# Performance work log

Measured on AMD Instinct MI355X. Metric: run time of the kernel, lower is better.

## Reference

```python
import jax, jax.numpy as jnp
import numpy as np

MODE_STATIC = 0
MODE_APPEARANCE_CHANGE = 2
MODE_BLINK = 3
MODE_AFFINE = 4


def _affine_warp(src, theta):
    """F.affine_grid + F.grid_sample(bilinear, zeros, align_corners=False).

    src:   [N, C, H, W]
    theta: [N, 2, 3]
    """
    N, C, H, W = src.shape
    dt = src.dtype
    # affine_grid base coords (align_corners=False): centers of pixels in [-1, 1]
    xs = (jnp.arange(W, dtype=dt) * 2 + 1) / W - 1  # [W]
    ys = (jnp.arange(H, dtype=dt) * 2 + 1) / H - 1  # [H]
    gx = (theta[:, 0, 0][:, None, None] * xs[None, None, :]
          + theta[:, 0, 1][:, None, None] * ys[None, :, None]
          + theta[:, 0, 2][:, None, None])  # [N, H, W]
    gy = (theta[:, 1, 0][:, None, None] * xs[None, None, :]
          + theta[:, 1, 1][:, None, None] * ys[None, :, None]
          + theta[:, 1, 2][:, None, None])  # [N, H, W]
    # unnormalize (align_corners=False)
    ix = ((gx + 1) * W - 1) / 2
    iy = ((gy + 1) * H - 1) / 2
    x0 = jnp.floor(ix)
    y0 = jnp.floor(iy)
    wx1 = ix - x0
    wy1 = iy - y0
    wx0 = 1 - wx1
    wy0 = 1 - wy1
    x0i = x0.astype(jnp.int32)
    y0i = y0.astype(jnp.int32)

    src_flat = src.reshape(N, C, H * W)

    def gather(xi, yi):
        valid = (xi >= 0) & (xi < W) & (yi >= 0) & (yi < H)  # zeros padding
        xi_c = jnp.clip(xi, 0, W - 1)
        yi_c = jnp.clip(yi, 0, H - 1)
        idx = (yi_c * W + xi_c).reshape(N, 1, H * W)
        v = jnp.take_along_axis(src_flat, idx, axis=2).reshape(N, C, H, W)
        return v * valid.astype(dt)[:, None]

    out = (gather(x0i, y0i) * (wx0 * wy0)[:, None]
           + gather(x0i + 1, y0i) * (wx1 * wy0)[:, None]
           + gather(x0i, y0i + 1) * (wx0 * wy1)[:, None]
           + gather(x0i + 1, y0i + 1) * (wx1 * wy1)[:, None])
    return out


def setup_inputs() -> dict:
    key = jax.random.key(0)
    ks = jax.random.split(key, 7)
    B, NI, C, H, W = 4, 16, 3, 256, 256
    g0 = jax.random.normal(ks[0], (B, NI, C, H, W), dtype=jnp.float32)
    m0 = jax.random.uniform(ks[1], (B, NI, 1, H, W), dtype=jnp.float32)
    mode_logits = jax.random.normal(ks[2], (B, NI, 5), dtype=jnp.float32)
    # near-identity affine transforms (realistic small motions)
    ident = jnp.array([1.0, 0.0, 0.0, 0.0, 1.0, 0.0], dtype=jnp.float32)
    transform_params = ident + 0.1 * jax.random.normal(ks[3], (B, NI, 6), dtype=jnp.float32)
    alpha = jax.random.uniform(ks[4], (B, NI, 1), dtype=jnp.float32)
    instance_valid = (jax.random.uniform(ks[5], (B, NI)) > 0.2).astype(jnp.float32)
    i_bg = jax.random.normal(ks[6], (B, C, H, W), dtype=jnp.float32)
    return {"g0": g0, "m0": m0, "mode_logits": mode_logits,
            "transform_params": transform_params, "alpha": alpha,
            "instance_valid": instance_valid, "i_bg": i_bg}


def reference(g0, m0, mode_logits, transform_params, alpha, instance_valid, i_bg):
    B, NI, C, H, W = g0.shape
    theta = transform_params.reshape(-1, 2, 3)  # [B*NI, 2, 3]
    warped_overlay = _affine_warp(g0.reshape(B * NI, C, H, W), theta).reshape(B, NI, C, H, W)
    warped_mask = _affine_warp(m0.reshape(B * NI, 1, H, W), theta).reshape(B, NI, 1, H, W)

    mode_ids = jnp.argmax(mode_logits, axis=-1)  # [B, NI]
    static_like = ((mode_ids == MODE_STATIC) | (mode_ids == MODE_APPEARANCE_CHANGE)
                   | (mode_ids == MODE_AFFINE)).astype(g0.dtype)[:, :, None, None, None]
    blink = (mode_ids == MODE_BLINK).astype(g0.dtype)[:, :, None, None, None]
    alpha_map = alpha[:, :, :, None, None]  # [B, NI, 1, 1, 1]
    valid = instance_valid[:, :, None, None, None]

    g_mid_per_instance = (static_like * warped_overlay + blink * warped_overlay * alpha_map) * valid
    m_mid_per_instance = (static_like * warped_mask + blink * warped_mask * alpha_map) * valid
    g_mid = g_mid_per_instance.sum(axis=1)
    m_mid = jnp.clip(m_mid_per_instance.sum(axis=1), 0.0, 1.0)
    i_base = i_bg + g_mid
    return (g_mid_per_instance, m_mid_per_instance, g_mid, m_mid, i_base)
```

## Files before the change

kernel.cpp:

```cpp
#include <hip/hip_runtime.h>
#include <hip/hip_bf16.h>

#define BB 4
#define NI 16
#define CC 3
#define HH 256
#define WW 256
#define HWSZ (HH * WW)

__global__ void prep_kernel(const float* __restrict__ mode_logits,
                            const float* __restrict__ tp,
                            const float* __restrict__ alpha,
                            const float* __restrict__ iv,
                            float* __restrict__ inst) {
    int i = threadIdx.x;
    if (i >= BB * NI) return;
    float best = mode_logits[i * 5];
    int bid = 0;
#pragma unroll
    for (int k = 1; k < 5; ++k) {
        float v = mode_logits[i * 5 + k];
        if (v > best) { best = v; bid = k; }
    }
    float coef;
    if (bid == 0 || bid == 2 || bid == 4)      coef = 1.0f;
    else if (bid == 3)                          coef = alpha[i];
    else                                        coef = 0.0f;
    coef *= iv[i];
#pragma unroll
    for (int k = 0; k < 6; ++k) inst[i * 8 + k] = tp[i * 6 + k];
    inst[i * 8 + 6] = coef;
    inst[i * 8 + 7] = 0.0f;
}

__global__ __launch_bounds__(256) void warp_main(
    const float* __restrict__ g0,
    const float* __restrict__ m0,
    const float* __restrict__ i_bg,
    const float* __restrict__ inst,
    float* __restrict__ out_gpi,
    float* __restrict__ out_mpi,
    float* __restrict__ out_gmid,
    float* __restrict__ out_mmid,
    float* __restrict__ out_ibase) {
    const int w = threadIdx.x;
    const int h = blockIdx.x;
    const int b = blockIdx.y;
    const int pix = h * WW + w;

    const float xs = (2 * w + 1) * (1.0f / WW) - 1.0f;
    const float ys = (2 * h + 1) * (1.0f / HH) - 1.0f;

    float acc[CC] = {0.f, 0.f, 0.f};
    float accm = 0.f;

    for (int ii = 0; ii < NI; ++ii) {
        const int id = b * NI + ii;
        const float* p = inst + id * 8;
        const float coef = p[6];

        float* gp = out_gpi + (size_t)id * CC * HWSZ + pix;
        float* mp = out_mpi + (size_t)id * HWSZ + pix;

        if (coef == 0.0f) {
            gp[0] = 0.0f; gp[HWSZ] = 0.0f; gp[2 * HWSZ] = 0.0f; mp[0] = 0.0f;
            continue;
        }

        const float gx = p[0] * xs + p[1] * ys + p[2];
        const float gy = p[3] * xs + p[4] * ys + p[5];
        const float ix = gx * (0.5f * WW) + (0.5f * WW - 0.5f);
        const float iy = gy * (0.5f * HH) + (0.5f * HH - 0.5f);
        const float x0f = floorf(ix), y0f = floorf(iy);
        const float wx1 = ix - x0f, wy1 = iy - y0f;
        const float wx0 = 1.0f - wx1, wy0 = 1.0f - wy1;
        const int x0 = (int)x0f, y0 = (int)y0f;
        const bool vx0 = (unsigned)x0 < (unsigned)WW;
        const bool vx1 = (unsigned)(x0 + 1) < (unsigned)WW;
        const bool vy0 = (unsigned)y0 < (unsigned)HH;
        const bool vy1 = (unsigned)(y0 + 1) < (unsigned)HH;
        const bool v00 = vx0 && vy0, v10 = vx1 && vy0;
        const bool v01 = vx0 && vy1, v11 = vx1 && vy1;
        const int o00 = y0 * WW + x0;
        const float w00 = wx0 * wy0, w10 = wx1 * wy0;
        const float w01 = wx0 * wy1, w11 = wx1 * wy1;

        const float* gsrc = g0 + (size_t)id * CC * HWSZ;
        const float* msrc = m0 + (size_t)id * HWSZ;

#pragma unroll
        for (int c = 0; c < CC; ++c) {
            const float* s = gsrc + c * HWSZ;
            const float a00 = v00 ? s[o00] : 0.0f;
            const float a10 = v10 ? s[o00 + 1] : 0.0f;
            const float a01 = v01 ? s[o00 + WW] : 0.0f;
            const float a11 = v11 ? s[o00 + WW + 1] : 0.0f;
            const float val = coef * (w00 * a00 + w10 * a10 + w01 * a01 + w11 * a11);
            gp[c * HWSZ] = val;
            acc[c] += val;
        }
        {
            const float a00 = v00 ? msrc[o00] : 0.0f;
            const float a10 = v10 ? msrc[o00 + 1] : 0.0f;
            const float a01 = v01 ? msrc[o00 + WW] : 0.0f;
            const float a11 = v11 ? msrc[o00 + WW + 1] : 0.0f;
            const float val = coef * (w00 * a00 + w10 * a10 + w01 * a01 + w11 * a11);
            mp[0] = val;
            accm += val;
        }
    }

    const int ob = b * CC * HWSZ + pix;
#pragma unroll
    for (int c = 0; c < CC; ++c) {
        out_gmid[ob + c * HWSZ] = acc[c];
        out_ibase[ob + c * HWSZ] = acc[c] + i_bg[ob + c * HWSZ];
    }
    out_mmid[b * HWSZ + pix] = fminf(fmaxf(accm, 0.0f), 1.0f);
}

extern "C" void kernel_launch(void* const* d_in, const int* in_sizes, int n_in,
                              void* d_out, int out_size, void* d_ws, size_t ws_size,
                              hipStream_t stream) {
    const float* g0          = (const float*)d_in[0];
    const float* m0          = (const float*)d_in[1];
    const float* mode_logits = (const float*)d_in[2];
    const float* tp          = (const float*)d_in[3];
    const float* alpha       = (const float*)d_in[4];
    const float* iv          = (const float*)d_in[5];
    const float* i_bg        = (const float*)d_in[6];

    float* out       = (float*)d_out;
    float* out_gpi   = out;
    float* out_mpi   = out_gpi  + (size_t)BB * NI * CC * HWSZ;
    float* out_gmid  = out_mpi  + (size_t)BB * NI * HWSZ;
    float* out_mmid  = out_gmid + (size_t)BB * CC * HWSZ;
    float* out_ibase = out_mmid + (size_t)BB * HWSZ;

    float* inst = (float*)d_ws;

    prep_kernel<<<1, 64, 0, stream>>>(mode_logits, tp, alpha, iv, inst);

    dim3 grid(HH, BB);
    warp_main<<<grid, WW, 0, stream>>>(g0, m0, i_bg, inst,
                                       out_gpi, out_mpi, out_gmid, out_mmid, out_ibase);
}
```

Before: 164.8 us.

## Split instance loop into two halves with partial sums and combine kernel

The per-batch instance loop is split across two grid z-slices, and each slice writes float4 partial sums to workspace. A separate combine kernel then adds the halves and produces g_mid, m_mid and i_base. The prep kernel now builds compacted lists of active instances, so the warp kernel skips zero-coefficient instances without branching per instance, and all gather loads are hoisted for more memory-level parallelism. This doubles the block count to improve occupancy, at the cost of an extra launch and partial-sum traffic; a fused fallback is kept for when workspace is too small.

```diff
diff --git a/kernel.cpp b/kernel.cpp
--- a/kernel.cpp
+++ b/kernel.cpp
@@ -1,5 +1,4 @@
 #include <hip/hip_runtime.h>
-#include <hip/hip_bf16.h>
 
 #define BB 4
 #define NI 16
@@ -7,65 +6,72 @@
 #define HH 256
 #define WW 256
 #define HWSZ (HH * WW)
-
-__global__ void prep_kernel(const float* __restrict__ mode_logits,
+#define HALF (NI / 2)
+
+
+__global__ void prep_kernel(const float* __restrict__ ml,
                             const float* __restrict__ tp,
-                            const float* __restrict__ alpha,
+                            const float* __restrict__ al,
                             const float* __restrict__ iv,
-                            float* __restrict__ inst) {
-    int i = threadIdx.x;
-    if (i >= BB * NI) return;
-    float best = mode_logits[i * 5];
+                            float* __restrict__ wsf) {
+    __shared__ float scoef[BB * NI];
+    const int i = threadIdx.x;
+    float best = ml[i * 5];
     int bid = 0;
 #pragma unroll
     for (int k = 1; k < 5; ++k) {
-        float v = mode_logits[i * 5 + k];
+        float v = ml[i * 5 + k];
         if (v > best) { best = v; bid = k; }
     }
-    float coef;
-    if (bid == 0 || bid == 2 || bid == 4)      coef = 1.0f;
-    else if (bid == 3)                          coef = alpha[i];
-    else                                        coef = 0.0f;
+    float coef = (bid == 0 || bid == 2 || bid == 4) ? 1.0f
+               : (bid == 3 ? al[i] : 0.0f);
     coef *= iv[i];
 #pragma unroll
-    for (int k = 0; k < 6; ++k) inst[i * 8 + k] = tp[i * 6 + k];
-    inst[i * 8 + 6] = coef;
-    inst[i * 8 + 7] = 0.0f;
-}
-
-__global__ __launch_bounds__(256) void warp_main(
+    for (int k = 0; k < 6; ++k) wsf[i * 8 + k] = tp[i * 6 + k];
+    wsf[i * 8 + 6] = coef;
+    wsf[i * 8 + 7] = 0.0f;
+    scoef[i] = coef;
+    __syncthreads();
+    if (i < BB * 2) {
+        const int b = i >> 1, half = i & 1;
+        int* wsi = (int*)(wsf + 512);
+        int cnt = 0;
+#pragma unroll
+        for (int k = 0; k < HALF; ++k) {
+            const int ii = half * HALF + k;
+            if (scoef[b * NI + ii] != 0.0f) wsi[8 + i * 8 + cnt++] = ii;
+        }
+        wsi[i] = cnt;
+    }
+}
+
+__global__ __launch_bounds__(256) void warp_half(
     const float* __restrict__ g0,
     const float* __restrict__ m0,
-    const float* __restrict__ i_bg,
-    const float* __restrict__ inst,
+    const float* __restrict__ wsf,
     float* __restrict__ out_gpi,
     float* __restrict__ out_mpi,
-    float* __restrict__ out_gmid,
-    float* __restrict__ out_mmid,
-    float* __restrict__ out_ibase) {
+    float* __restrict__ part) {
     const int w = threadIdx.x;
     const int h = blockIdx.x;
     const int b = blockIdx.y;
+    const int half = blockIdx.z;
     const int pix = h * WW + w;
 
     const float xs = (2 * w + 1) * (1.0f / WW) - 1.0f;
     const float ys = (2 * h + 1) * (1.0f / HH) - 1.0f;
 
-    float acc[CC] = {0.f, 0.f, 0.f};
-    float accm = 0.f;
-
-    for (int ii = 0; ii < NI; ++ii) {
+    const int* wsi = (const int*)(wsf + 512);
+    const int lk = b * 2 + half;
+    const int nact = wsi[lk];
+    const int* act = wsi + 8 + lk * 8;
+
+    float acc0 = 0.f, acc1 = 0.f, acc2 = 0.f, accm = 0.f;
+
+    auto proc = [&](int ii) {
         const int id = b * NI + ii;
-        const float* p = inst + id * 8;
+        const float* p = wsf + id * 8;
         const float coef = p[6];
-
-        float* gp = out_gpi + (size_t)id * CC * HWSZ + pix;
-        float* mp = out_mpi + (size_t)id * HWSZ + pix;
-
-        if (coef == 0.0f) {
-            gp[0] = 0.0f; gp[HWSZ] = 0.0f; gp[2 * HWSZ] = 0.0f; mp[0] = 0.0f;
-            continue;
-        }
 
         const float gx = p[0] * xs + p[1] * ys + p[2];
         const float gy = p[3] * xs + p[4] * ys + p[5];
@@ -87,29 +93,122 @@
 
         const float* gsrc = g0 + (size_t)id * CC * HWSZ;
         const float* msrc = m0 + (size_t)id * HWSZ;
-
+        float* gp = out_gpi + (size_t)id * CC * HWSZ + pix;
+
+        const float a00_0 = v00 ? gsrc[o00] : 0.0f;
+        const float a10_0 = v10 ? gsrc[o00 + 1] : 0.0f;
+        const float a01_0 = v01 ? gsrc[o00 + WW] : 0.0f;
+        const float a11_0 = v11 ? gsrc[o00 + WW + 1] : 0.0f;
+        const float a00_1 = v00 ? gsrc[HWSZ + o00] : 0.0f;
+        const float a10_1 = v10 ? gsrc[HWSZ + o00 + 1] : 0.0f;
+        const float a01_1 = v01 ? gsrc[HWSZ + o00 + WW] : 0.0f;
+        const float a11_1 = v11 ? gsrc[HWSZ + o00 + WW + 1] : 0.0f;
+        const float a00_2 = v00 ? gsrc[2 * HWSZ + o00] : 0.0f;
+        const float a10_2 = v10 ? gsrc[2 * HWSZ + o00 + 1] : 0.0f;
+        const float a01_2 = v01 ? gsrc[2 * HWSZ + o00 + WW] : 0.0f;
+        const float a11_2 = v11 ? gsrc[2 * HWSZ + o00 + WW + 1] : 0.0f;
+        const float m00 = v00 ? msrc[o00] : 0.0f;
+        const float m10 = v10 ? msrc[o00 + 1] : 0.0f;
+        const float m01 = v01 ? msrc[o00 + WW] : 0.0f;
+        const float m11 = v11 ? msrc[o00 + WW + 1] : 0.0f;
+
+        const float val0 = coef * (w00 * a00_0 + w10 * a10_0 + w01 * a01_0 + w11 * a11_0);
+        const float val1 = coef * (w00 * a00_1 + w10 * a10_1 + w01 * a01_1 + w11 * a11_1);
+        const float val2 = coef * (w00 * a00_2 + w10 * a10_2 + w01 * a01_2 + w11 * a11_2);
+        const float valm = coef * (w00 * m00 + w10 * m10 + w01 * m01 + w11 * m11);
+
+        gp[0] = val0; gp[HWSZ] = val1; gp[2 * HWSZ] = val2;
+        out_mpi[(size_t)id * HWSZ + pix] = valm;
+        acc0 += val0; acc1 += val1; acc2 += val2; accm += valm;
+    };
+
+    int k = 0;
+    for (; k + 2 <= nact; k += 2) { proc(act[k]); proc(act[k + 1]); }
+    if (k < nact) proc(act[k]);
+
+#pragma unroll
+    for (int kk = 0; kk < HALF; ++kk) {
+        const int ii = half * HALF + kk;
+        const int id = b * NI + ii;
+        if (wsf[id * 8 + 6] == 0.0f) {
+            float* gp = out_gpi + (size_t)id * CC * HWSZ + pix;
+            gp[0] = 0.0f; gp[HWSZ] = 0.0f; gp[2 * HWSZ] = 0.0f;
+            out_mpi[(size_t)id * HWSZ + pix] = 0.0f;
+        }
+    }
+
+    float4 pv; pv.x = acc0; pv.y = acc1; pv.z = acc2; pv.w = accm;
+    ((float4*)part)[(size_t)(half * BB + b) * HWSZ + pix] = pv;
+}
+
+__global__ __launch_bounds__(256) void combine_k(
+    const float* __restrict__ part,
+    const float* __restrict__ i_bg,
+    float* __restrict__ out_gmid,
+    float* __restrict__ out_mmid,
+    float* __restrict__ out_ibase) {
+    const int w = threadIdx.x;
+    const int h = blockIdx.x;
+    const int b = blockIdx.y;
+    const int pix = h * WW + w;
+    const float4 p0 = ((const float4*)part)[(size_t)b * HWSZ + pix];
+    const float4 p1 = ((const float4*)part)[(size_t)(BB + b) * HWSZ + pix];
+    const float s0 = p0.x + p1.x, s1 = p0.y + p1.y, s2 = p0.z + p1.z;
+    const float sm = p0.w + p1.w;
+    const int ob = b * CC * HWSZ + pix;
+    out_gmid[ob] = s0;
+    out_gmid[ob + HWSZ] = s1;
+    out_gmid[ob + 2 * HWSZ] = s2;
+    out_ibase[ob] = s0 + i_bg[ob];
+    out_ibase[ob + HWSZ] = s1 + i_bg[ob + HWSZ];
+    out_ibase[ob + 2 * HWSZ] = s2 + i_bg[ob + 2 * HWSZ];
+    out_mmid[b * HWSZ + pix] = fminf(fmaxf(sm, 0.0f), 1.0f);
+}
+
+__global__ __launch_bounds__(256) void warp_fused(
+    const float* __restrict__ g0, const float* __restrict__ m0,
+    const float* __restrict__ i_bg, const float* __restrict__ inst,
+    float* __restrict__ out_gpi, float* __restrict__ out_mpi,
+    float* __restrict__ out_gmid, float* __restrict__ out_mmid,
+    float* __restrict__ out_ibase) {
+    const int w = threadIdx.x, h = blockIdx.x, b = blockIdx.y;
+    const int pix = h * WW + w;
+    const float xs = (2 * w + 1) * (1.0f / WW) - 1.0f;
+    const float ys = (2 * h + 1) * (1.0f / HH) - 1.0f;
+    float acc[CC] = {0.f, 0.f, 0.f}; float accm = 0.f;
+    for (int ii = 0; ii < NI; ++ii) {
+        const int id = b * NI + ii;
+        const float* p = inst + id * 8;
+        const float coef = p[6];
+        float* gp = out_gpi + (size_t)id * CC * HWSZ + pix;
+        float* mp = out_mpi + (size_t)id * HWSZ + pix;
+        if (coef == 0.0f) { gp[0] = 0.f; gp[HWSZ] = 0.f; gp[2 * HWSZ] = 0.f; mp[0] = 0.f; continue; }
+        const float gx = p[0] * xs + p[1] * ys + p[2];
+        const float gy = p[3] * xs + p[4] * ys + p[5];
+        const float ix = gx * (0.5f * WW) + (0.5f * WW - 0.5f);
+        const float iy = gy * (0.5f * HH) + (0.5f * HH - 0.5f);
+        const float x0f = floorf(ix), y0f = floorf(iy);
+        const float wx1 = ix - x0f, wy1 = iy - y0f;
+        const float wx0 = 1.0f - wx1, wy0 = 1.0f - wy1;
+        const int x0 = (int)x0f, y0 = (int)y0f;
+        const bool vx0 = (unsigned)x0 < (unsigned)WW, vx1 = (unsigned)(x0 + 1) < (unsigned)WW;
+        const bool vy0 = (unsigned)y0 < (unsigned)HH, vy1 = (unsigned)(y0 + 1) < (unsigned)HH;
+        const bool v00 = vx0 && vy0, v10 = vx1 && vy0, v01 = vx0 && vy1, v11 = vx1 && vy1;
+        const int o00 = y0 * WW + x0;
+        const float w00 = wx0 * wy0, w10 = wx1 * wy0, w01 = wx0 * wy1, w11 = wx1 * wy1;
+        const float* gsrc = g0 + (size_t)id * CC * HWSZ;
+        const float* msrc = m0 + (size_t)id * HWSZ;
 #pragma unroll
         for (int c = 0; c < CC; ++c) {
             const float* s = gsrc + c * HWSZ;
-            const float a00 = v00 ? s[o00] : 0.0f;
-            const float a10 = v10 ? s[o00 + 1] : 0.0f;
-            const float a01 = v01 ? s[o00 + WW] : 0.0f;
-            const float a11 = v11 ? s[o00 + WW + 1] : 0.0f;
-            const float val = coef * (w00 * a00 + w10 * a10 + w01 * a01 + w11 * a11);
-            gp[c * HWSZ] = val;
-            acc[c] += val;
+            const float val = coef * (w00 * (v00 ? s[o00] : 0.f) + w10 * (v10 ? s[o00 + 1] : 0.f)
+                                    + w01 * (v01 ? s[o00 + WW] : 0.f) + w11 * (v11 ? s[o00 + WW + 1] : 0.f));
+            gp[c * HWSZ] = val; acc[c] += val;
         }
-        {
-            const float a00 = v00 ? msrc[o00] : 0.0f;
-            const float a10 = v10 ? msrc[o00 + 1] : 0.0f;
-            const float a01 = v01 ? msrc[o00 + WW] : 0.0f;
-            const float a11 = v11 ? msrc[o00 + WW + 1] : 0.0f;
-            const float val = coef * (w00 * a00 + w10 * a10 + w01 * a01 + w11 * a11);
-            mp[0] = val;
-            accm += val;
-        }
-    }
-
+        const float valm = coef * (w00 * (v00 ? msrc[o00] : 0.f) + w10 * (v10 ? msrc[o00 + 1] : 0.f)
+                                 + w01 * (v01 ? msrc[o00 + WW] : 0.f) + w11 * (v11 ? msrc[o00 + WW + 1] : 0.f));
+        mp[0] = valm; accm += valm;
+    }
     const int ob = b * CC * HWSZ + pix;
 #pragma unroll
     for (int c = 0; c < CC; ++c) {
@@ -137,11 +236,20 @@
     float* out_mmid  = out_gmid + (size_t)BB * CC * HWSZ;
     float* out_ibase = out_mmid + (size_t)BB * HWSZ;
 
-    float* inst = (float*)d_ws;
-
-    prep_kernel<<<1, 64, 0, stream>>>(mode_logits, tp, alpha, iv, inst);
-
-    dim3 grid(HH, BB);
-    warp_main<<<grid, WW, 0, stream>>>(g0, m0, i_bg, inst,
-                                       out_gpi, out_mpi, out_gmid, out_mmid, out_ibase);
-}
+    float* wsf  = (float*)d_ws;
+    float* part = wsf + 1024;
+    const size_t need = 4096 + (size_t)2 * BB * HWSZ * 4 * sizeof(float);
+
+    prep_kernel<<<1, 64, 0, stream>>>(mode_logits, tp, alpha, iv, wsf);
+
+    if (ws_size >= need) {
+        dim3 grid(HH, BB, 2);
+        warp_half<<<grid, WW, 0, stream>>>(g0, m0, wsf, out_gpi, out_mpi, part);
+        dim3 grid2(HH, BB);
+        combine_k<<<grid2, WW, 0, stream>>>(part, i_bg, out_gmid, out_mmid, out_ibase);
+    } else {
+        dim3 grid(HH, BB);
+        warp_fused<<<grid, WW, 0, stream>>>(g0, m0, i_bg, wsf, out_gpi, out_mpi,
+                                            out_gmid, out_mmid, out_ibase);
+    }
+}
```

Measured after the change: 157.6 us. 1.05x faster.

## Split warp into per-instance kernel plus separate reduction kernel

Applied to the files above, without the earlier changes.

The fused kernel, which looped over all 16 instances per pixel and launched only 1024 blocks, is split into two kernels. The first warps each instance in its own block (16x more blocks) and issues all 16 gathers up front. The second re-reads the per-instance outputs to compute the sums, the clamped mask and i_base. This raises parallelism and memory-level parallelism, but the ~67MB of per-instance output has to be read back from memory a second time, and there is an extra launch.

```diff
diff --git a/kernel.cpp b/kernel.cpp
--- a/kernel.cpp
+++ b/kernel.cpp
@@ -1,5 +1,4 @@
 #include <hip/hip_runtime.h>
-#include <hip/hip_bf16.h>
 
 #define BB 4
 #define NI 16
@@ -8,38 +7,102 @@
 #define WW 256
 #define HWSZ (HH * WW)
 
-__global__ void prep_kernel(const float* __restrict__ mode_logits,
+__global__ void prep_kernel(const float* __restrict__ ml,
                             const float* __restrict__ tp,
-                            const float* __restrict__ alpha,
+                            const float* __restrict__ al,
                             const float* __restrict__ iv,
-                            float* __restrict__ inst) {
-    int i = threadIdx.x;
+                            float* __restrict__ wsf) {
+    const int i = threadIdx.x;
     if (i >= BB * NI) return;
-    float best = mode_logits[i * 5];
+    float best = ml[i * 5];
     int bid = 0;
 #pragma unroll
     for (int k = 1; k < 5; ++k) {
-        float v = mode_logits[i * 5 + k];
+        float v = ml[i * 5 + k];
         if (v > best) { best = v; bid = k; }
     }
-    float coef;
-    if (bid == 0 || bid == 2 || bid == 4)      coef = 1.0f;
-    else if (bid == 3)                          coef = alpha[i];
-    else                                        coef = 0.0f;
+    float coef = (bid == 0 || bid == 2 || bid == 4) ? 1.0f
+               : (bid == 3 ? al[i] : 0.0f);
     coef *= iv[i];
 #pragma unroll
-    for (int k = 0; k < 6; ++k) inst[i * 8 + k] = tp[i * 6 + k];
-    inst[i * 8 + 6] = coef;
-    inst[i * 8 + 7] = 0.0f;
+    for (int k = 0; k < 6; ++k) wsf[i * 8 + k] = tp[i * 6 + k];
+    wsf[i * 8 + 6] = coef;
+    wsf[i * 8 + 7] = 0.0f;
 }
 
-__global__ __launch_bounds__(256) void warp_main(
+__global__ __launch_bounds__(256) void warp_inst(
     const float* __restrict__ g0,
     const float* __restrict__ m0,
+    const float* __restrict__ wsf,
+    float* __restrict__ out_gpi,
+    float* __restrict__ out_mpi) {
+    const int w = threadIdx.x;
+    const int h = blockIdx.x;
+    const int id = blockIdx.y;
+    const int pix = h * WW + w;
+
+    const float* p = wsf + id * 8;
+    const float coef = p[6];
+
+    float* gp = out_gpi + (size_t)id * CC * HWSZ + pix;
+    float* mp = out_mpi + (size_t)id * HWSZ + pix;
+
+    if (coef == 0.0f) {
+        gp[0] = 0.0f; gp[HWSZ] = 0.0f; gp[2 * HWSZ] = 0.0f; mp[0] = 0.0f;
+        return;
+    }
+
+    const float xs = (2 * w + 1) * (1.0f / WW) - 1.0f;
+    const float ys = (2 * h + 1) * (1.0f / HH) - 1.0f;
+
+    const float gx = p[0] * xs + p[1] * ys + p[2];
+    const float gy = p[3] * xs + p[4] * ys + p[5];
+    const float ix = gx * (0.5f * WW) + (0.5f * WW - 0.5f);
+    const float iy = gy * (0.5f * HH) + (0.5f * HH - 0.5f);
+    const float x0f = floorf(ix), y0f = floorf(iy);
+    const float wx1 = ix - x0f, wy1 = iy - y0f;
+    const float wx0 = 1.0f - wx1, wy0 = 1.0f - wy1;
+    const int x0 = (int)x0f, y0 = (int)y0f;
+    const bool vx0 = (unsigned)x0 < (unsigned)WW;
+    const bool vx1 = (unsigned)(x0 + 1) < (unsigned)WW;
+    const bool vy0 = (unsigned)y0 < (unsigned)HH;
+    const bool vy1 = (unsigned)(y0 + 1) < (unsigned)HH;
+    const bool v00 = vx0 && vy0, v10 = vx1 && vy0;
+    const bool v01 = vx0 && vy1, v11 = vx1 && vy1;
+    const int o00 = y0 * WW + x0;
+    const float w00 = wx0 * wy0, w10 = wx1 * wy0;
+    const float w01 = wx0 * wy1, w11 = wx1 * wy1;
+
+    const float* gsrc = g0 + (size_t)id * CC * HWSZ;
+    const float* msrc = m0 + (size_t)id * HWSZ;
+
+    const float a00_0 = v00 ? gsrc[o00] : 0.0f;
+    const float a10_0 = v10 ? gsrc[o00 + 1] : 0.0f;
+    const float a01_0 = v01 ? gsrc[o00 + WW] : 0.0f;
+    const float a11_0 = v11 ? gsrc[o00 + WW + 1] : 0.0f;
+    const float a00_1 = v00 ? gsrc[HWSZ + o00] : 0.0f;
+    const float a10_1 = v10 ? gsrc[HWSZ + o00 + 1] : 0.0f;
+    const float a01_1 = v01 ? gsrc[HWSZ + o00 + WW] : 0.0f;
+    const float a11_1 = v11 ? gsrc[HWSZ + o00 + WW + 1] : 0.0f;
+    const float a00_2 = v00 ? gsrc[2 * HWSZ + o00] : 0.0f;
+    const float a10_2 = v10 ? gsrc[2 * HWSZ + o00 + 1] : 0.0f;
+    const float a01_2 = v01 ? gsrc[2 * HWSZ + o00 + WW] : 0.0f;
+    const float a11_2 = v11 ? gsrc[2 * HWSZ + o00 + WW + 1] : 0.0f;
+    const float m00 = v00 ? msrc[o00] : 0.0f;
+    const float m10 = v10 ? msrc[o00 + 1] : 0.0f;
+    const float m01 = v01 ? msrc[o00 + WW] : 0.0f;
+    const float m11 = v11 ? msrc[o00 + WW + 1] : 0.0f;
+
+    gp[0]        = coef * (w00 * a00_0 + w10 * a10_0 + w01 * a01_0 + w11 * a11_0);
+    gp[HWSZ]     = coef * (w00 * a00_1 + w10 * a10_1 + w01 * a01_1 + w11 * a11_1);
+    gp[2 * HWSZ] = coef * (w00 * a00_2 + w10 * a10_2 + w01 * a01_2 + w11 * a11_2);
+    mp[0]        = coef * (w00 * m00 + w10 * m10 + w01 * m01 + w11 * m11);
+}
+
+__global__ __launch_bounds__(256) void combine_k(
+    const float* __restrict__ gpi,
+    const float* __restrict__ mpi,
     const float* __restrict__ i_bg,
-    const float* __restrict__ inst,
-    float* __restrict__ out_gpi,
-    float* __restrict__ out_mpi,
     float* __restrict__ out_gmid,
     float* __restrict__ out_mmid,
     float* __restrict__ out_ibase) {
@@ -48,75 +111,23 @@
     const int b = blockIdx.y;
     const int pix = h * WW + w;
 
-    const float xs = (2 * w + 1) * (1.0f / WW) - 1.0f;
-    const float ys = (2 * h + 1) * (1.0f / HH) - 1.0f;
-
-    float acc[CC] = {0.f, 0.f, 0.f};
-    float accm = 0.f;
-
+    float s0 = 0.f, s1 = 0.f, s2 = 0.f, sm = 0.f;
+#pragma unroll
     for (int ii = 0; ii < NI; ++ii) {
-        const int id = b * NI + ii;
-        const float* p = inst + id * 8;
-        const float coef = p[6];
-
-        float* gp = out_gpi + (size_t)id * CC * HWSZ + pix;
-        float* mp = out_mpi + (size_t)id * HWSZ + pix;
-
-        if (coef == 0.0f) {
-            gp[0] = 0.0f; gp[HWSZ] = 0.0f; gp[2 * HWSZ] = 0.0f; mp[0] = 0.0f;
-            continue;
-        }
-
-        const float gx = p[0] * xs + p[1] * ys + p[2];
-        const float gy = p[3] * xs + p[4] * ys + p[5];
-        const float ix = gx * (0.5f * WW) + (0.5f * WW - 0.5f);
-        const float iy = gy * (0.5f * HH) + (0.5f * HH - 0.5f);
-        const float x0f = floorf(ix), y0f = floorf(iy);
-        const float wx1 = ix - x0f, wy1 = iy - y0f;
-        const float wx0 = 1.0f - wx1, wy0 = 1.0f - wy1;
-        const int x0 = (int)x0f, y0 = (int)y0f;
-        const bool vx0 = (unsigned)x0 < (unsigned)WW;
-        const bool vx1 = (unsigned)(x0 + 1) < (unsigned)WW;
-        const bool vy0 = (unsigned)y0 < (unsigned)HH;
-        const bool vy1 = (unsigned)(y0 + 1) < (unsigned)HH;
-        const bool v00 = vx0 && vy0, v10 = vx1 && vy0;
-        const bool v01 = vx0 && vy1, v11 = vx1 && vy1;
-        const int o00 = y0 * WW + x0;
-        const float w00 = wx0 * wy0, w10 = wx1 * wy0;
-        const float w01 = wx0 * wy1, w11 = wx1 * wy1;
-
-        const float* gsrc = g0 + (size_t)id * CC * HWSZ;
-        const float* msrc = m0 + (size_t)id * HWSZ;
-
-#pragma unroll
-        for (int c = 0; c < CC; ++c) {
-            const float* s = gsrc + c * HWSZ;
-            const float a00 = v00 ? s[o00] : 0.0f;
-            const float a10 = v10 ? s[o00 + 1] : 0.0f;
-            const float a01 = v01 ? s[o00 + WW] : 0.0f;
-            const float a11 = v11 ? s[o00 + WW + 1] : 0.0f;
-            const float val = coef * (w00 * a00 + w10 * a10 + w01 * a01 + w11 * a11);
-            gp[c * HWSZ] = val;
-            acc[c] += val;
-        }
-        {
-            const float a00 = v00 ? msrc[o00] : 0.0f;
-            const float a10 = v10 ? msrc[o00 + 1] : 0.0f;
-            const float a01 = v01 ? msrc[o00 + WW] : 0.0f;
-            const float a11 = v11 ? msrc[o00 + WW + 1] : 0.0f;
-            const float val = coef * (w00 * a00 + w10 * a10 + w01 * a01 + w11 * a11);
-            mp[0] = val;
-            accm += val;
-        }
+        const size_t gb = (size_t)(b * NI + ii) * CC * HWSZ + pix;
+        s0 += gpi[gb];
+        s1 += gpi[gb + HWSZ];
+        s2 += gpi[gb + 2 * HWSZ];
+        sm += mpi[(size_t)(b * NI + ii) * HWSZ + pix];
     }
-
     const int ob = b * CC * HWSZ + pix;
-#pragma unroll
-    for (int c = 0; c < CC; ++c) {
-        out_gmid[ob + c * HWSZ] = acc[c];
-        out_ibase[ob + c * HWSZ] = acc[c] + i_bg[ob + c * HWSZ];
-    }
-    out_mmid[b * HWSZ + pix] = fminf(fmaxf(accm, 0.0f), 1.0f);
+    out_gmid[ob] = s0;
+    out_gmid[ob + HWSZ] = s1;
+    out_gmid[ob + 2 * HWSZ] = s2;
+    out_ibase[ob] = s0 + i_bg[ob];
+    out_ibase[ob + HWSZ] = s1 + i_bg[ob + HWSZ];
+    out_ibase[ob + 2 * HWSZ] = s2 + i_bg[ob + 2 * HWSZ];
+    out_mmid[b * HWSZ + pix] = fminf(fmaxf(sm, 0.0f), 1.0f);
 }
 
 extern "C" void kernel_launch(void* const* d_in, const int* in_sizes, int n_in,
@@ -137,11 +148,14 @@
     float* out_mmid  = out_gmid + (size_t)BB * CC * HWSZ;
     float* out_ibase = out_mmid + (size_t)BB * HWSZ;
 
-    float* inst = (float*)d_ws;
+    float* wsf = (float*)d_ws;
 
-    prep_kernel<<<1, 64, 0, stream>>>(mode_logits, tp, alpha, iv, inst);
+    prep_kernel<<<1, 64, 0, stream>>>(mode_logits, tp, alpha, iv, wsf);
 
-    dim3 grid(HH, BB);
-    warp_main<<<grid, WW, 0, stream>>>(g0, m0, i_bg, inst,
-                                       out_gpi, out_mpi, out_gmid, out_mmid, out_ibase);
+    dim3 grid1(HH, BB * NI);
+    warp_inst<<<grid1, WW, 0, stream>>>(g0, m0, wsf, out_gpi, out_mpi);
+
+    dim3 grid2(HH, BB);
+    combine_k<<<grid2, WW, 0, stream>>>(out_gpi, out_mpi, i_bg,
+                                        out_gmid, out_mmid, out_ibase);
 }
```

After: 156.4 us. -5.1%, faster.
